# Optimization experiments

Measured on AMD Instinct MI355X. Metric: run time of the kernel, lower is better.

Reference implementation:

```python
import jax, jax.numpy as jnp
import numpy as np

N_USERS = 50000
N_ENTITIES = 250000
N_RELATIONS = 24
EMBED_DIM = 128
RELATION_DIM = 128
KG_BATCH = 16384
KG_L2_LAMBDA = 1e-5


def _l2_loss_mean(x):
    # mean over batch of (||x||^2 / 2)
    return jnp.mean(jnp.sum(x * x, axis=1) / 2.0)


def setup_inputs() -> dict:
    key = jax.random.key(0)
    k1, k2, k3, k4, k5, k6, k7 = jax.random.split(key, 7)
    n_total = N_ENTITIES + N_USERS
    # xavier-uniform-like init scale
    s_e = float(np.sqrt(6.0 / (n_total + EMBED_DIM)))
    s_r = float(np.sqrt(6.0 / (N_RELATIONS + RELATION_DIM)))
    s_m = float(np.sqrt(6.0 / (EMBED_DIM + RELATION_DIM)))
    entity_user_embed = jax.random.uniform(k1, (n_total, EMBED_DIM), jnp.float32, -s_e, s_e)
    relation_embed = jax.random.uniform(k2, (N_RELATIONS, RELATION_DIM), jnp.float32, -s_r, s_r)
    trans_M = jax.random.uniform(k3, (N_RELATIONS, EMBED_DIM, RELATION_DIM), jnp.float32, -s_m, s_m)
    h = jax.random.randint(k4, (KG_BATCH,), 0, n_total, dtype=jnp.int64 if jax.config.jax_enable_x64 else jnp.int32)
    r = jax.random.randint(k5, (KG_BATCH,), 0, N_RELATIONS, dtype=h.dtype)
    pos_t = jax.random.randint(k6, (KG_BATCH,), 0, n_total, dtype=h.dtype)
    neg_t = jax.random.randint(k7, (KG_BATCH,), 0, n_total, dtype=h.dtype)
    return {
        "entity_user_embed": entity_user_embed,
        "relation_embed": relation_embed,
        "trans_M": trans_M,
        "h": h,
        "r": r,
        "pos_t": pos_t,
        "neg_t": neg_t,
    }


def reference(entity_user_embed, relation_embed, trans_M, h, r, pos_t, neg_t):
    # KGAT.calc_kg_loss (mode='train_kg')
    r_embed = relation_embed[r]            # [B, R]
    W_r = trans_M[r]                       # [B, E, R] per-edge TransR matrix (gather)
    h_embed = entity_user_embed[h]         # [B, E]
    pos_t_embed = entity_user_embed[pos_t] # [B, E]
    neg_t_embed = entity_user_embed[neg_t] # [B, E]

    # bmm([B,1,E], [B,E,R]) -> [B,R]
    r_mul_h = jnp.einsum('be,ber->br', h_embed, W_r)
    r_mul_pos_t = jnp.einsum('be,ber->br', pos_t_embed, W_r)
    r_mul_neg_t = jnp.einsum('be,ber->br', neg_t_embed, W_r)

    pos_score = jnp.sum(jnp.square(r_mul_h + r_embed - r_mul_pos_t), axis=1)
    neg_score = jnp.sum(jnp.square(r_mul_h + r_embed - r_mul_neg_t), axis=1)

    kg_loss = jnp.mean(-jax.nn.log_sigmoid(neg_score - pos_score))
    l2_loss = (_l2_loss_mean(r_mul_h) + _l2_loss_mean(r_embed)
               + _l2_loss_mean(r_mul_pos_t) + _l2_loss_mean(r_mul_neg_t))
    return kg_loss + KG_L2_LAMBDA * l2_loss
```

## Files before the change

kernel.cpp:

```cpp
#include <hip/hip_runtime.h>
#include <math.h>

#define KG_B    16384
#define KG_D    128
#define KG_NR   24
#define KG_TM   32
#define KG_BPAD (KG_B + KG_NR * KG_TM)
#define KG_NGRP (KG_BPAD / KG_TM)
#define KG_HB   16

#define WS_BSUM     KG_BPAD
#define WS_CNTPART  (KG_BPAD + KG_NGRP)
#define WS_PREW_BYTES 131072

typedef __attribute__((ext_vector_type(8))) short bf16x8;
typedef __attribute__((ext_vector_type(4))) float f32x4;

__device__ __forceinline__ unsigned bf16r(float f) {
    return (__float_as_uint(f) + 0x8000u) >> 16;
}
__device__ __forceinline__ unsigned pack2(float lo, float hi) {
    return bf16r(lo) | (bf16r(hi) << 16);
}

__global__ __launch_bounds__(1024) void kg_hist_prep(const int* __restrict__ r,
                                                     const float* __restrict__ M,
                                                     int* __restrict__ perm,
                                                     int* __restrict__ cntpart,
                                                     unsigned short* __restrict__ preW) {
    const int t = threadIdx.x;

    if (blockIdx.x >= KG_HB) {
        __shared__ __align__(16) unsigned short sWp[KG_D * KG_D];
        const int k  = blockIdx.x - KG_HB;
        const int e  = t >> 3;
        const int c0 = (t & 7) * 16;
        const float* src = M + ((size_t)k << 14) + (size_t)e * KG_D + c0;
        float4 rw[4];
#pragma unroll
        for (int f = 0; f < 4; ++f) rw[f] = ((const float4*)src)[f];
#pragma unroll
        for (int dc = 0; dc < 16; ++dc) {
            const int col = c0 + dc;
            const float v = ((const float*)&rw[0])[dc];
            sWp[col * KG_D + e] = (unsigned short)bf16r(v);
        }
        __syncthreads();
        uint4* dst = (uint4*)(preW + ((size_t)k << 14));
        const uint4* s4 = (const uint4*)sWp;
        dst[2 * t]     = s4[2 * t];
        dst[2 * t + 1] = s4[2 * t + 1];
        return;
    }

    __shared__ int hc[24];
    const int j = blockIdx.x;
    if (t < 24) hc[t] = 0;
    for (int i = j * 1024 + t; i < KG_BPAD; i += KG_HB * 1024) perm[i] = -1;
    __syncthreads();
    atomicAdd(&hc[r[j * 1024 + t]], 1);
    __syncthreads();
    if (t < 24) cntpart[j * 32 + t] = hc[t];
}

__global__ __launch_bounds__(1024) void kg_scatter(const int* __restrict__ r,
                                                   const int* __restrict__ cntpart,
                                                   int* __restrict__ perm) {
    __shared__ int wcnt[16][25];
    __shared__ int wbase[16][25];
    __shared__ int tot[24], myb[24], pb0[24];

    const int j    = blockIdx.x;
    const int t    = threadIdx.x;
    const int w    = t >> 6;
    const int lane = t & 63;

    const int k = r[j * 1024 + t];

    unsigned long long mym = 0;
#pragma unroll
    for (int b = 0; b < 24; ++b) {
        const unsigned long long m = __ballot(k == b);
        if (k == b) mym = m;
        if (lane == 0) wcnt[w][b] = (int)__popcll(m);
    }
    const int rank_w = (int)__popcll(mym & ((1ull << lane) - 1ull));
    __syncthreads();

    if (t < 24) {
        int s = 0;
        for (int w2 = 0; w2 < 16; ++w2) { wbase[w2][t] = s; s += wcnt[w2][t]; }
        int s2 = 0, mb = 0;
        for (int j2 = 0; j2 < KG_HB; ++j2) {
            const int c = cntpart[j2 * 32 + t];
            s2 += c;
            if (j2 < j) mb += c;
        }
        tot[t] = s2;
        myb[t] = mb;
    }
    __syncthreads();
    if (t == 0) {
        int run = 0;
        for (int k2 = 0; k2 < 24; ++k2) {
            pb0[k2] = run;
            run += (tot[k2] + (KG_TM - 1)) & ~(KG_TM - 1);
        }
    }
    __syncthreads();

    const int pos = pb0[k] + myb[k] + wbase[w][k] + rank_w;
    perm[pos] = j * 1024 + t;
}

__global__ __launch_bounds__(256, 3) void kg_main(
    const float* __restrict__ ent, const float* __restrict__ rel,
    const unsigned short* __restrict__ preW,
    const int* __restrict__ h,     const int* __restrict__ r,
    const int* __restrict__ pt,    const int* __restrict__ nt,
    const int* __restrict__ perm,  float* __restrict__ bsum)
{
    __shared__ __align__(16) unsigned short sX[3 * KG_TM * KG_D];
    __shared__ float sScr[2][KG_TM][4];

    const int tid   = threadIdx.x;
    const int slot0 = blockIdx.x * KG_TM;
    const int p0    = perm[slot0];
    if (p0 < 0) {
        if (tid == 0) bsum[blockIdx.x] = 0.f;
        return;
    }
    const int rb = __builtin_amdgcn_readfirstlane(r[p0]);

    const int l   = tid & 63;
    const int wv  = tid >> 6;
    const int rt  = wv & 1;
    const int chs = wv >> 1;
    const int li  = l & 15;
    const int kq  = l >> 4;

    const unsigned short* __restrict__ preWk = preW + ((size_t)rb << 14);
    bf16x8 bpre[4][4];
#pragma unroll
    for (int kk = 0; kk < 4; ++kk)
#pragma unroll
        for (int n = 0; n < 4; ++n)
            bpre[kk][n] = *(const bf16x8*)&preWk[(chs * 64 + n * 16 + li) * KG_D
                                                 + kk * 32 + kq * 8];
    const float* relrow = rel + (size_t)rb * KG_D + chs * 64;
    float relv[4];
#pragma unroll
    for (int n = 0; n < 4; ++n) relv[n] = relrow[n * 16 + li];

    {
        const int g  = tid >> 3;
        const int e0 = (tid & 7) * 16;
        const int pg = perm[slot0 + g];
        const int bb = pg < 0 ? p0 : pg;
        const int idx3[3] = { h[bb], pt[bb], nt[bb] };
        const int sw = (g & 7) << 3;
#pragma unroll
        for (int t3 = 0; t3 < 3; ++t3) {
            const float* src = ent + (size_t)idx3[t3] * KG_D + e0;
            const float4 f0 = ((const float4*)src)[0];
            const float4 f1 = ((const float4*)src)[1];
            const float4 f2 = ((const float4*)src)[2];
            const float4 f3 = ((const float4*)src)[3];
            uint4 u0, u1;
            u0.x = pack2(f0.x, f0.y); u0.y = pack2(f0.z, f0.w);
            u0.z = pack2(f1.x, f1.y); u0.w = pack2(f1.z, f1.w);
            u1.x = pack2(f2.x, f2.y); u1.y = pack2(f2.z, f2.w);
            u1.z = pack2(f3.x, f3.y); u1.w = pack2(f3.z, f3.w);
            unsigned short* base = sX + t3 * (KG_TM * KG_D) + g * KG_D;
            *(uint4*)(base + ((e0    ) ^ sw)) = u0;
            *(uint4*)(base + ((e0 + 8) ^ sw)) = u1;
        }
    }
    __syncthreads();

    const int ar  = rt * 16 + li;
    const int asw = (ar & 7) << 3;

    f32x4 accf[3][4];
#pragma unroll
    for (int t3 = 0; t3 < 3; ++t3)
#pragma unroll
        for (int n = 0; n < 4; ++n) accf[t3][n] = (f32x4)0.f;

#pragma unroll
    for (int kk = 0; kk < 4; ++kk) {
        const int e0 = kk * 32 + kq * 8;
        bf16x8 af[3];
#pragma unroll
        for (int t3 = 0; t3 < 3; ++t3)
            af[t3] = *(const bf16x8*)&sX[t3 * (KG_TM * KG_D) + ar * KG_D + (e0 ^ asw)];
#pragma unroll
        for (int n = 0; n < 4; ++n) {
            accf[0][n] = __builtin_amdgcn_mfma_f32_16x16x32_bf16(af[0], bpre[kk][n], accf[0][n], 0, 0, 0);
            accf[1][n] = __builtin_amdgcn_mfma_f32_16x16x32_bf16(af[1], bpre[kk][n], accf[1][n], 0, 0, 0);
            accf[2][n] = __builtin_amdgcn_mfma_f32_16x16x32_bf16(af[2], bpre[kk][n], accf[2][n], 0, 0, 0);
        }
    }

    float ps[4] = {0,0,0,0}, ns[4] = {0,0,0,0}, sq[4] = {0,0,0,0};
#pragma unroll
    for (int n = 0; n < 4; ++n) {
        const float rv = relv[n];
#pragma unroll
        for (int j = 0; j < 4; ++j) {
            const float va = accf[0][n][j];
            const float vp = accf[1][n][j];
            const float vn = accf[2][n][j];
            const float s  = va + rv;
            const float dp = s - vp;
            const float dn = s - vn;
            ps[j] += dp * dp;
            ns[j] += dn * dn;
            sq[j] += va * va + vp * vp + vn * vn + rv * rv;
        }
    }
#pragma unroll
    for (int j = 0; j < 4; ++j)
#pragma unroll
        for (int m = 1; m < 16; m <<= 1) {
            ps[j] += __shfl_xor(ps[j], m);
            ns[j] += __shfl_xor(ns[j], m);
            sq[j] += __shfl_xor(sq[j], m);
        }

    if (li == 0) {
#pragma unroll
        for (int j = 0; j < 4; ++j) {
            const int row = rt * 16 + kq * 4 + j;
            sScr[chs][row][0] = ps[j];
            sScr[chs][row][1] = ns[j];
            sScr[chs][row][2] = sq[j];
        }
    }
    __syncthreads();

    if (tid < 64) {
        float term = 0.f;
        if (tid < KG_TM) {
            const int row = tid;
            const float P = sScr[0][row][0] + sScr[1][row][0];
            const float N = sScr[0][row][1] + sScr[1][row][1];
            const float S = sScr[0][row][2] + sScr[1][row][2];
            const int pg = perm[slot0 + row];
            if (pg >= 0) {
                const float x = P - N;
                term = fmaxf(x, 0.f) + log1pf(expf(-fabsf(x)))
                     + 5e-6f * S;
            }
        }
#pragma unroll
        for (int off = 16; off > 0; off >>= 1) term += __shfl_down(term, off);
        if (tid == 0) bsum[blockIdx.x] = term;
    }
}

__global__ __launch_bounds__(256) void kg_final(const float* __restrict__ bsum,
                                                float* __restrict__ out) {
    __shared__ float s[256];
    const int t = threadIdx.x;
    float acc = 0.f;
    for (int i = t; i < KG_NGRP; i += 256) acc += bsum[i];
    s[t] = acc;
    __syncthreads();
    for (int off = 128; off > 0; off >>= 1) {
        if (t < off) s[t] += s[t + off];
        __syncthreads();
    }
    if (t == 0) out[0] = s[0] * (1.0f / (float)KG_B);
}

extern "C" void kernel_launch(void* const* d_in, const int* in_sizes, int n_in,
                              void* d_out, int out_size, void* d_ws, size_t ws_size,
                              hipStream_t stream) {
    const float* ent = (const float*)d_in[0];
    const float* rel = (const float*)d_in[1];
    const float* M   = (const float*)d_in[2];
    const int*   h   = (const int*)d_in[3];
    const int*   r   = (const int*)d_in[4];
    const int*   pt  = (const int*)d_in[5];
    const int*   nt  = (const int*)d_in[6];

    int*            perm    = (int*)d_ws;
    float*          bsum    = (float*)d_ws + WS_BSUM;
    int*            cntpart = (int*)d_ws + WS_CNTPART;
    unsigned short* preW    = (unsigned short*)((char*)d_ws + WS_PREW_BYTES);
    float*          out     = (float*)d_out;

    kg_hist_prep<<<KG_HB + KG_NR, 1024, 0, stream>>>(r, M, perm, cntpart, preW);
    kg_scatter  <<<KG_HB, 1024, 0, stream>>>(r, cntpart, perm);
    kg_main     <<<KG_NGRP, 256, 0, stream>>>(ent, rel, preW, h, r, pt, nt, perm, bsum);
    kg_final    <<<1, 256, 0, stream>>>(bsum, out);
}
```

Measured before the change: 27.87 us.

## Fuse histogram and scatter into one sort kernel, pre-sort gather indices

Merges the histogram and scatter kernels into a single launch: each of the 16 sort blocks recomputes the full relation histogram redundantly from r via wave ballots, then scatters. The scatter also writes relation-sorted copies of h/pos_t/neg_t indices plus a per-segment relation id, so the main kernel loads indices contiguously instead of through a perm indirection. This removes one kernel launch and a dependent global read chain, at the cost of redundant histogram work per block and extra index writes.

```diff
diff --git a/kernel.cpp b/kernel.cpp
--- a/kernel.cpp
+++ b/kernel.cpp
@@ -9,9 +9,12 @@
 #define KG_NGRP (KG_BPAD / KG_TM)
 #define KG_HB   16
 
-#define WS_BSUM     KG_BPAD
-#define WS_CNTPART  (KG_BPAD + KG_NGRP)
-#define WS_PREW_BYTES 131072
+#define WS_BSUM   KG_BPAD
+#define WS_SEGREL (KG_BPAD + KG_NGRP)
+#define WS_HS     (KG_BPAD + 2 * KG_NGRP)
+#define WS_PS     (WS_HS + KG_BPAD)
+#define WS_NS     (WS_PS + KG_BPAD)
+#define WS_PREW_BYTES 393216
 
 typedef __attribute__((ext_vector_type(8))) short bf16x8;
 typedef __attribute__((ext_vector_type(4))) float f32x4;
@@ -23,11 +26,14 @@
     return bf16r(lo) | (bf16r(hi) << 16);
 }
 
-__global__ __launch_bounds__(1024) void kg_hist_prep(const int* __restrict__ r,
-                                                     const float* __restrict__ M,
-                                                     int* __restrict__ perm,
-                                                     int* __restrict__ cntpart,
-                                                     unsigned short* __restrict__ preW) {
+__global__ __launch_bounds__(1024) void kg_sort_prep(
+    const int* __restrict__ r,   const float* __restrict__ M,
+    const int* __restrict__ h,   const int* __restrict__ pt,
+    const int* __restrict__ nt,
+    int* __restrict__ perm,      int* __restrict__ segrel,
+    int* __restrict__ hS,        int* __restrict__ pS,
+    int* __restrict__ nS,        unsigned short* __restrict__ preW)
+{
     const int t = threadIdx.x;
 
     if (blockIdx.x >= KG_HB) {
@@ -53,46 +59,34 @@
         return;
     }
 
-    __shared__ int hc[24];
-    const int j = blockIdx.x;
-    if (t < 24) hc[t] = 0;
-    for (int i = j * 1024 + t; i < KG_BPAD; i += KG_HB * 1024) perm[i] = -1;
-    __syncthreads();
-    atomicAdd(&hc[r[j * 1024 + t]], 1);
-    __syncthreads();
-    if (t < 24) cntpart[j * 32 + t] = hc[t];
-}
-
-__global__ __launch_bounds__(1024) void kg_scatter(const int* __restrict__ r,
-                                                   const int* __restrict__ cntpart,
-                                                   int* __restrict__ perm) {
+    __shared__ int cnt[16][25];
     __shared__ int wcnt[16][25];
     __shared__ int wbase[16][25];
     __shared__ int tot[24], myb[24], pb0[24];
+    __shared__ int padtot_s;
 
     const int j    = blockIdx.x;
-    const int t    = threadIdx.x;
     const int w    = t >> 6;
     const int lane = t & 63;
 
-    const int k = r[j * 1024 + t];
-
-    unsigned long long mym = 0;
-#pragma unroll
-    for (int b = 0; b < 24; ++b) {
-        const unsigned long long m = __ballot(k == b);
-        if (k == b) mym = m;
-        if (lane == 0) wcnt[w][b] = (int)__popcll(m);
-    }
-    const int rank_w = (int)__popcll(mym & ((1ull << lane) - 1ull));
+    {
+        int acc = 0;
+        for (int it = 0; it < 16; ++it) {
+            const int k = r[w * 1024 + it * 64 + lane];
+#pragma unroll
+            for (int b = 0; b < 24; ++b) {
+                const unsigned long long m = __ballot(k == b);
+                if (lane == b) acc += (int)__popcll(m);
+            }
+        }
+        if (lane < 24) cnt[w][lane] = acc;
+    }
     __syncthreads();
 
     if (t < 24) {
-        int s = 0;
-        for (int w2 = 0; w2 < 16; ++w2) { wbase[w2][t] = s; s += wcnt[w2][t]; }
         int s2 = 0, mb = 0;
         for (int j2 = 0; j2 < KG_HB; ++j2) {
-            const int c = cntpart[j2 * 32 + t];
+            const int c = cnt[j2][t];
             s2 += c;
             if (j2 < j) mb += c;
         }
@@ -106,18 +100,56 @@
             pb0[k2] = run;
             run += (tot[k2] + (KG_TM - 1)) & ~(KG_TM - 1);
         }
+        padtot_s = run;
+    }
+    __syncthreads();
+
+    const int elem = j * 1024 + t;
+    const int k = r[elem];
+    unsigned long long mym = 0;
+#pragma unroll
+    for (int b = 0; b < 24; ++b) {
+        const unsigned long long m = __ballot(k == b);
+        if (k == b) mym = m;
+        if (lane == 0) wcnt[w][b] = (int)__popcll(m);
+    }
+    const int rank_w = (int)__popcll(mym & ((1ull << lane) - 1ull));
+    __syncthreads();
+    if (t < 24) {
+        int s = 0;
+        for (int w2 = 0; w2 < 16; ++w2) { wbase[w2][t] = s; s += wcnt[w2][t]; }
     }
     __syncthreads();
 
     const int pos = pb0[k] + myb[k] + wbase[w][k] + rank_w;
-    perm[pos] = j * 1024 + t;
+    perm[pos] = elem;
+    hS[pos]   = h[elem];
+    pS[pos]   = pt[elem];
+    nS[pos]   = nt[elem];
+    if ((pos & (KG_TM - 1)) == 0) segrel[pos >> 5] = k;
+
+    if (j == 0) {
+        if (t < 24) {
+            const int e0 = pb0[t] + tot[t];
+            const int e1 = pb0[t] + ((tot[t] + (KG_TM - 1)) & ~(KG_TM - 1));
+            for (int p = e0; p < e1; ++p) {
+                perm[p] = -1; hS[p] = 0; pS[p] = 0; nS[p] = 0;
+            }
+        }
+        const int padtot = padtot_s;
+        for (int i = padtot + t; i < KG_BPAD; i += 1024) {
+            perm[i] = -1; hS[i] = 0; pS[i] = 0; nS[i] = 0;
+        }
+        for (int g = (padtot >> 5) + t; g < KG_NGRP; g += 1024)
+            segrel[g] = -1;
+    }
 }
 
 __global__ __launch_bounds__(256, 3) void kg_main(
     const float* __restrict__ ent, const float* __restrict__ rel,
     const unsigned short* __restrict__ preW,
-    const int* __restrict__ h,     const int* __restrict__ r,
-    const int* __restrict__ pt,    const int* __restrict__ nt,
+    const int* __restrict__ hS,    const int* __restrict__ pS,
+    const int* __restrict__ nS,    const int* __restrict__ segrel,
     const int* __restrict__ perm,  float* __restrict__ bsum)
 {
     __shared__ __align__(16) unsigned short sX[3 * KG_TM * KG_D];
@@ -125,12 +157,11 @@
 
     const int tid   = threadIdx.x;
     const int slot0 = blockIdx.x * KG_TM;
-    const int p0    = perm[slot0];
-    if (p0 < 0) {
+    const int rb    = __builtin_amdgcn_readfirstlane(segrel[blockIdx.x]);
+    if (rb < 0) {
         if (tid == 0) bsum[blockIdx.x] = 0.f;
         return;
     }
-    const int rb = __builtin_amdgcn_readfirstlane(r[p0]);
 
     const int l   = tid & 63;
     const int wv  = tid >> 6;
@@ -155,9 +186,7 @@
     {
         const int g  = tid >> 3;
         const int e0 = (tid & 7) * 16;
-        const int pg = perm[slot0 + g];
-        const int bb = pg < 0 ? p0 : pg;
-        const int idx3[3] = { h[bb], pt[bb], nt[bb] };
+        const int idx3[3] = { hS[slot0 + g], pS[slot0 + g], nS[slot0 + g] };
         const int sw = (g & 7) << 3;
 #pragma unroll
         for (int t3 = 0; t3 < 3; ++t3) {
@@ -246,8 +275,7 @@
             const float P = sScr[0][row][0] + sScr[1][row][0];
             const float N = sScr[0][row][1] + sScr[1][row][1];
             const float S = sScr[0][row][2] + sScr[1][row][2];
-            const int pg = perm[slot0 + row];
-            if (pg >= 0) {
+            if (perm[slot0 + row] >= 0) {
                 const float x = P - N;
                 term = fmaxf(x, 0.f) + log1pf(expf(-fabsf(x)))
                      + 5e-6f * S;
@@ -285,14 +313,18 @@
     const int*   pt  = (const int*)d_in[5];
     const int*   nt  = (const int*)d_in[6];
 
-    int*            perm    = (int*)d_ws;
-    float*          bsum    = (float*)d_ws + WS_BSUM;
-    int*            cntpart = (int*)d_ws + WS_CNTPART;
-    unsigned short* preW    = (unsigned short*)((char*)d_ws + WS_PREW_BYTES);
-    float*          out     = (float*)d_out;
-
-    kg_hist_prep<<<KG_HB + KG_NR, 1024, 0, stream>>>(r, M, perm, cntpart, preW);
-    kg_scatter  <<<KG_HB, 1024, 0, stream>>>(r, cntpart, perm);
-    kg_main     <<<KG_NGRP, 256, 0, stream>>>(ent, rel, preW, h, r, pt, nt, perm, bsum);
+    int*            perm   = (int*)d_ws;
+    float*          bsum   = (float*)d_ws + WS_BSUM;
+    int*            segrel = (int*)d_ws + WS_SEGREL;
+    int*            hS     = (int*)d_ws + WS_HS;
+    int*            pS     = (int*)d_ws + WS_PS;
+    int*            nS     = (int*)d_ws + WS_NS;
+    unsigned short* preW   = (unsigned short*)((char*)d_ws + WS_PREW_BYTES);
+    float*          out    = (float*)d_out;
+
+    kg_sort_prep<<<KG_HB + KG_NR, 1024, 0, stream>>>(r, M, h, pt, nt,
+                                                     perm, segrel, hS, pS, nS, preW);
+    kg_main     <<<KG_NGRP, 256, 0, stream>>>(ent, rel, preW, hS, pS, nS,
+                                              segrel, perm, bsum);
     kg_final    <<<1, 256, 0, stream>>>(bsum, out);
 }
```

Result: slower. 36.81 us (+32.1%).
